# Kernel optimization log

Measured on AMD Instinct MI355X. Metric: run time of the kernel, lower is better.

## Reference

```python
import jax, jax.numpy as jnp
import numpy as np

DIM = 512
HEADS = 8
DIM_HEAD = 64
DIM_INNER = HEADS * DIM_HEAD
FRAC_GRAD = 0.5
SCALE = DIM_HEAD ** -0.5
EPS_CUMPROD = 1e-10
EPS_INV = 1e-8


def setup_inputs() -> dict:
    key = jax.random.key(0)
    ks = jax.random.split(key, 8)
    b, n = 2, 2048
    x = jax.random.normal(ks[0], (b, n, DIM), dtype=jnp.float32)
    gamma = jnp.ones((DIM,), dtype=jnp.float32)
    w_qkv = jax.random.normal(ks[1], (DIM, 3 * DIM_INNER), dtype=jnp.float32) * 0.02
    b_qkv = jnp.zeros((3 * DIM_INNER,), dtype=jnp.float32)
    # to_a: torch init is zeros weight + bias 10; use small random weight and
    # moderate bias so the decay gate is non-trivial for correctness testing
    w_a = jax.random.normal(ks[2], (DIM, DIM_INNER), dtype=jnp.float32) * 0.02
    b_a = jnp.full((DIM_INNER,), 2.0, dtype=jnp.float32)
    w_out = jax.random.normal(ks[3], (DIM_INNER, DIM), dtype=jnp.float32) * 0.02
    b_out = jnp.zeros((DIM,), dtype=jnp.float32)
    return {"x": x, "gamma": gamma, "w_qkv": w_qkv, "b_qkv": b_qkv,
            "w_a": w_a, "b_a": b_a, "w_out": w_out, "b_out": b_out}


def _rms_norm(x, gamma):
    # F.normalize(x, dim=-1) * sqrt(dim) * gamma
    nrm = jnp.linalg.norm(x, axis=-1, keepdims=True)
    return x / jnp.maximum(nrm, 1e-12) * (DIM ** 0.5) * gamma


def _safe_cumprod(t, axis):
    t = jnp.clip(t, EPS_CUMPROD, 1.0)
    return jnp.exp(jnp.cumsum(jnp.log(t), axis=axis))


def reference(x, gamma, w_qkv, b_qkv, w_a, b_a, w_out, b_out):
    b, n, _ = x.shape
    x = _rms_norm(x, gamma)

    qkv = x @ w_qkv + b_qkv  # [b, n, 3*h*d]
    qkv = qkv.reshape(b, n, 3, HEADS, DIM_HEAD).transpose(2, 0, 3, 1, 4)  # [3,b,h,n,d]
    q, k, v = qkv[0], qkv[1], qkv[2]
    q = q * SCALE

    # data-dependent relative-position decay gate
    a = (x @ w_a + b_a).reshape(b, n, HEADS, DIM_HEAD).transpose(0, 2, 1, 3)  # [b,h,n,d]
    a = a * FRAC_GRAD + jax.lax.stop_gradient(a) * (1.0 - FRAC_GRAD)
    a = jax.nn.sigmoid(a)
    a_cum = _safe_cumprod(a, axis=-2)
    a_cum_inv = 1.0 / jnp.maximum(a_cum, EPS_INV)

    q = q * a_cum
    k = k * a_cum_inv

    sim = jnp.einsum('bhid,bhjd->bhij', q, k)
    causal_mask = jnp.triu(jnp.ones((n, n), dtype=bool), k=1)
    attn = jnp.where(causal_mask, 0.0, sim)  # no softmax in decay branch

    out = jnp.einsum('bhij,bhjd->bhid', attn, v)  # [b,h,n,d]
    out = out.transpose(0, 2, 1, 3).reshape(b, n, DIM_INNER)
    return out @ w_out + b_out
```

## Files before the change

kernel.cpp:

```cpp
#include <hip/hip_runtime.h>
#include <hip/hip_cooperative_groups.h>


namespace cg = cooperative_groups;

using s8v   = __attribute__((ext_vector_type(8))) short;
using f32x4 = __attribute__((ext_vector_type(4))) float;

__device__ __forceinline__ unsigned short f2b(float f) {
  unsigned int u = __builtin_bit_cast(unsigned int, f);
  u += 0x7FFFu + ((u >> 16) & 1u);
  return (unsigned short)(u >> 16);
}
__device__ __forceinline__ float b2f(unsigned short b) {
  unsigned int u = ((unsigned int)b) << 16;
  return __builtin_bit_cast(float, u);
}
__device__ __forceinline__ f32x4 mfma16(s8v a, s8v b, f32x4 c) {
  return __builtin_amdgcn_mfma_f32_16x16x32_bf16(a, b, c, 0, 0, 0);
}
__device__ __forceinline__ void gload16(const void* g, void* l) {
  __builtin_amdgcn_global_load_lds(
      (const __attribute__((address_space(1))) void*)g,
      (__attribute__((address_space(3))) void*)l, 16, 0, 0);
}

__device__ __forceinline__ void st_prep(int u, int tid, char* arena,
    const float* __restrict__ x, const float* __restrict__ gamma,
    short* __restrict__ xnb,
    const float* __restrict__ w_qkv, const float* __restrict__ w_a,
    const float* __restrict__ w_out,
    short* __restrict__ wT, short* __restrict__ woT) {
  int lane = tid & 63, wave = tid >> 6;
  if (u < 1024) {
    int row = u * 4 + wave;
    const float4* xp = reinterpret_cast<const float4*>(x + (size_t)row * 512 + lane * 8);
    float4 v0 = xp[0], v1 = xp[1];
    float ss = v0.x*v0.x + v0.y*v0.y + v0.z*v0.z + v0.w*v0.w
             + v1.x*v1.x + v1.y*v1.y + v1.z*v1.z + v1.w*v1.w;
#pragma unroll
    for (int off = 32; off > 0; off >>= 1) ss += __shfl_xor(ss, off, 64);
    float s = 22.627416997969522f / fmaxf(sqrtf(ss), 1e-12f);
    const float* g = gamma + lane * 8;
    float vals[8] = {v0.x, v0.y, v0.z, v0.w, v1.x, v1.y, v1.z, v1.w};
    s8v o;
#pragma unroll
    for (int j = 0; j < 8; ++j) o[j] = (short)f2b(vals[j] * s * g[j]);
    *reinterpret_cast<s8v*>(xnb + (size_t)row * 512 + lane * 8) = o;
  } else {
    float (*t)[33] = reinterpret_cast<float (*)[33]>(arena);
    int id = u - 1024;
    int bx = id % 80, k0 = (id / 80) * 32;
    const float* src; short* dst; int N, n0;
    if (bx < 48)      { src = w_qkv; dst = wT;                      N = 1536; n0 = bx * 32; }
    else if (bx < 64) { src = w_a;   dst = wT + (size_t)1536 * 512; N = 512;  n0 = (bx - 48) * 32; }
    else              { src = w_out; dst = woT;                     N = 512;  n0 = (bx - 64) * 32; }
    int tx = tid & 31, ty = tid >> 5;
    __syncthreads();
#pragma unroll
    for (int i = 0; i < 4; ++i)
      t[ty + 8 * i][tx] = src[(size_t)(k0 + ty + 8 * i) * N + n0 + tx];
    __syncthreads();
#pragma unroll
    for (int i = 0; i < 4; ++i)
      dst[(size_t)(n0 + ty + 8 * i) * 512 + k0 + tx] = (short)f2b(t[tx][ty + 8 * i]);
  }
}

template <int BM, int BN, int FM, int FN>
__device__ __forceinline__ void gemm_core(const short* __restrict__ A,
                                          const short* __restrict__ Bm,
                                          char* LA, char* LB,
                                          int m0, int n0, int tid,
                                          f32x4 (&acc)[FM][FN]) {
  const int lane = tid & 63, wave = tid >> 6;
  const int wr = (wave >> 1) * (BM / 2), wc = (wave & 1) * (BN / 2);
#pragma unroll 1
  for (int t = 0; t < 8; ++t) {
    const int k0 = t * 64;
#pragma unroll
    for (int r = 0; r < BM / 32; ++r) {
      int o = r * 4096 + tid * 16;
      int row = o >> 7;
      int ce = (((o & 127) ^ ((row & 7) << 4)) >> 1);
      gload16(A + (size_t)(m0 + row) * 512 + k0 + ce, LA + o);
    }
#pragma unroll
    for (int r = 0; r < BN / 32; ++r) {
      int o = r * 4096 + tid * 16;
      int row = o >> 7;
      int ce = (((o & 127) ^ ((row & 7) << 4)) >> 1);
      gload16(Bm + (size_t)(n0 + row) * 512 + k0 + ce, LB + o);
    }
    __syncthreads();
#pragma unroll
    for (int kk = 0; kk < 2; ++kk) {
      s8v af[FM], bf[FN];
#pragma unroll
      for (int m = 0; m < FM; ++m) {
        int row = wr + m * 16 + (lane & 15);
        int ad = ((row << 7) + kk * 64 + ((lane >> 4) << 4)) ^ ((row & 7) << 4);
        af[m] = *reinterpret_cast<const s8v*>(LA + ad);
      }
#pragma unroll
      for (int n = 0; n < FN; ++n) {
        int row = wc + n * 16 + (lane & 15);
        int ad = ((row << 7) + kk * 64 + ((lane >> 4) << 4)) ^ ((row & 7) << 4);
        bf[n] = *reinterpret_cast<const s8v*>(LB + ad);
      }
#pragma unroll
      for (int m = 0; m < FM; ++m)
#pragma unroll
        for (int n = 0; n < FN; ++n)
          acc[m][n] = mfma16(af[m], bf[n], acc[m][n]);
    }
    if (t + 1 < 8) __syncthreads();
  }
}

__device__ __forceinline__ void st_gemm0(int vid, int tid, char* arena,
    const short* __restrict__ xnb, const short* __restrict__ wT,
    short* __restrict__ qkvb, const float* __restrict__ b_qkv,
    const float* __restrict__ b_a, float* __restrict__ araw,
    float* __restrict__ csum) {
  const int lane = tid & 63, wave = tid >> 6;
  int xcd = vid & 7, rq = vid >> 3;
  int bx = rq & 15, by = xcd * 4 + (rq >> 4);
  int m0 = by * 128, n0 = bx * 128;
  f32x4 acc[4][4] = {};
  gemm_core<128, 128, 4, 4>(xnb, wT, arena, arena + 16384, m0, n0, tid, acc);
  int wr = (wave >> 1) * 64, wc = (wave & 1) * 64;
  if (n0 < 1536) {
#pragma unroll
    for (int m = 0; m < 4; ++m)
#pragma unroll
      for (int n = 0; n < 4; ++n)
#pragma unroll
        for (int r = 0; r < 4; ++r) {
          int row = m0 + wr + m * 16 + ((lane >> 4) << 2) + r;
          int col = n0 + wc + n * 16 + (lane & 15);
          float v = acc[m][n][r] + b_qkv[col];
          int w = col >> 9, h = (col >> 6) & 7, d = col & 63;
          int b = row >> 11, nn = row & 2047;
          qkvb[((((size_t)(w * 2 + b)) * 8 + h) * 2048 + nn) * 64 + d] = (short)f2b(v);
        }
  } else {
    float cs[4] = {};
    int b = m0 >> 11;
#pragma unroll
    for (int m = 0; m < 4; ++m)
#pragma unroll
      for (int n = 0; n < 4; ++n)
#pragma unroll
        for (int r = 0; r < 4; ++r) {
          int row = m0 + wr + m * 16 + ((lane >> 4) << 2) + r;
          int gc = n0 + wc + n * 16 + (lane & 15) - 1536;
          int h = gc >> 6, d = gc & 63, nn = row & 2047;
          float xv = acc[m][n][r] + b_a[gc];
          araw[((size_t)(b * 8 + h) * 2048 + nn) * 64 + d] = xv;
          float a = 1.f / (1.f + expf(-xv));
          a = fminf(fmaxf(a, 1e-10f), 1.f);
          cs[n] += logf(a);
        }
#pragma unroll
    for (int n = 0; n < 4; ++n) {
      cs[n] += __shfl_xor(cs[n], 16, 64);
      cs[n] += __shfl_xor(cs[n], 32, 64);
    }
    int nsel = lane >> 4;
    float v = (nsel == 0) ? cs[0] : (nsel == 1) ? cs[1] : (nsel == 2) ? cs[2] : cs[3];
    int col = wc + nsel * 16 + (lane & 15);
    int gc = n0 + col - 1536;
    int h = gc >> 6, d = gc & 63;
    int chunkg = ((m0 & 2047) >> 6) + (wave >> 1);
    csum[(((size_t)(b * 8 + h)) * 32 + chunkg) * 64 + d] = v;
  }
}

__device__ __forceinline__ float csum_prefix(const float* __restrict__ csum,
                                             int bh, int chunk, int d) {
  float pre = 0.f;
#pragma unroll
  for (int c = 0; c < 32; ++c) {
    float cv = csum[((size_t)bh * 32 + c) * 64 + d];
    pre += (c < chunk) ? cv : 0.f;
  }
  return pre;
}

__device__ __forceinline__ void st_scan2(int vid, int tid, char* arena,
    const short* __restrict__ qkvb, const float* __restrict__ araw,
    const float* __restrict__ csum, short* __restrict__ q2,
    short* __restrict__ k2, short* __restrict__ vT, short* __restrict__ Sbuf) {
  int chunk = vid & 31, bh = vid >> 5;
  int lane = tid & 63, wave = tid >> 6, d = lane;
  short (*kL)[64] = reinterpret_cast<short (*)[64]>(arena);
  short (*vL)[64] = reinterpret_cast<short (*)[64]>(arena + 8192);
  char* kT  = arena + 16384;
  char* vTl = arena + 24576;
  float (*wsum)[64] = reinterpret_cast<float (*)[64]>(arena + 16384);
  float pre = csum_prefix(csum, bh, chunk, d);
  const float* ap = araw + ((size_t)bh * 2048 + chunk * 64 + wave * 16) * 64 + d;
  float la[16]; float run = 0.f;
#pragma unroll
  for (int rr = 0; rr < 16; ++rr) {
    float xv = ap[rr * 64];
    float a = 1.f / (1.f + expf(-xv));
    a = fminf(fmaxf(a, 1e-10f), 1.f);
    run += logf(a);
    la[rr] = run;
  }
  wsum[wave][d] = run;
  __syncthreads();
#pragma unroll
  for (int w = 0; w < 3; ++w) if (w < wave) pre += wsum[w][d];
  const size_t WS = (size_t)2 * 8 * 2048 * 64;
  size_t base = ((size_t)bh * 2048 + chunk * 64 + wave * 16) * 64 + d;
#pragma unroll 4
  for (int rr = 0; rr < 16; ++rr) {
    int r = wave * 16 + rr;
    float g = expf(pre + la[rr]);
    float gi = 1.f / fmaxf(g, 1e-8f);
    float qv = b2f((unsigned short)qkvb[base + rr * 64]);
    float kv = b2f((unsigned short)qkvb[base + WS + rr * 64]);
    short vb = qkvb[base + 2 * WS + rr * 64];
    q2[base + rr * 64] = (short)f2b(qv * 0.125f * g);
    unsigned short kb = f2b(kv * gi);
    k2[base + rr * 64] = (short)kb;
    kL[r][d] = (short)kb;
    vL[r][d] = vb;
  }
  __syncthreads();
  short* vTrow = vT + ((size_t)bh * 64 + d) * 2048 + chunk * 64;
#pragma unroll
  for (int gg = 0; gg < 2; ++gg) {
    int g8 = wave + gg * 4;
    s8v pk, pv;
#pragma unroll
    for (int j = 0; j < 8; ++j) { pk[j] = kL[g8 * 8 + j][d]; pv[j] = vL[g8 * 8 + j][d]; }
    *reinterpret_cast<s8v*>(vTrow + g8 * 8) = pv;
    int ad = ((d << 7) + g8 * 16) ^ ((d & 7) << 4);
    *reinterpret_cast<s8v*>(kT  + ad) = pk;
    *reinterpret_cast<s8v*>(vTl + ad) = pv;
  }
  __syncthreads();
  f32x4 acc[4] = {};
#pragma unroll
  for (int kk = 0; kk < 2; ++kk) {
    int arow = wave * 16 + (lane & 15);
    int aad = ((arow << 7) + kk * 64 + ((lane >> 4) << 4)) ^ ((arow & 7) << 4);
    s8v av = *reinterpret_cast<const s8v*>(vTl + aad);
#pragma unroll
    for (int n = 0; n < 4; ++n) {
      int brow = n * 16 + (lane & 15);
      int bad = ((brow << 7) + kk * 64 + ((lane >> 4) << 4)) ^ ((brow & 7) << 4);
      acc[n] = mfma16(av, *reinterpret_cast<const s8v*>(kT + bad), acc[n]);
    }
  }
  short* Sp = Sbuf + ((size_t)bh * 32 + chunk) * 4096;
#pragma unroll
  for (int n = 0; n < 4; ++n)
#pragma unroll
    for (int r = 0; r < 4; ++r)
      Sp[(wave * 16 + ((lane >> 4) << 2) + r) * 64 + n * 16 + (lane & 15)] = (short)f2b(acc[n][r]);
}

__device__ __forceinline__ void st_sprefix(int vid, int tid,
    const short* __restrict__ Sbuf, short* __restrict__ Spre) {
  int bh = vid >> 4;
  int e = ((vid & 15) << 8) + tid;
  size_t base = (size_t)bh * 32 * 4096 + e;
  unsigned short v[32];
#pragma unroll
  for (int c = 0; c < 32; ++c)
    v[c] = (unsigned short)Sbuf[base + (size_t)c * 4096];
  float acc = 0.f;
#pragma unroll
  for (int c = 0; c < 32; ++c) {
    Spre[base + (size_t)c * 4096] = (short)f2b(acc);
    acc += b2f(v[c]);
  }
}

__device__ __forceinline__ void st_attnk(int vid, int tid, char* arena,
    const short* __restrict__ q2, const short* __restrict__ k2,
    const short* __restrict__ vT, const short* __restrict__ Spre,
    short* __restrict__ aout) {
  int chunk = vid & 31, bh = vid >> 5;
  int lane = tid & 63, wave = tid >> 6;
  char* LQ = arena;
  char* LK = arena + 8192;
  char* LV = arena + 16384;
  char* LS = arena + 24576;
#pragma unroll
  for (int rr = 0; rr < 2; ++rr) {
    int o = rr * 4096 + tid * 16;
    int row = o >> 7;
    int ce = (((o & 127) ^ ((row & 7) << 4)) >> 1);
    gload16(q2   + ((size_t)bh * 2048 + chunk * 64 + row) * 64 + ce, LQ + o);
    gload16(k2   + ((size_t)bh * 2048 + chunk * 64 + row) * 64 + ce, LK + o);
    gload16(vT   + ((size_t)bh * 64 + row) * 2048 + chunk * 64 + ce, LV + o);
    gload16(Spre + (((size_t)bh * 32 + chunk) * 64 + row) * 64 + ce, LS + o);
  }
  __syncthreads();
  f32x4 accS[4] = {}, accO[4] = {};
#pragma unroll
  for (int kk = 0; kk < 2; ++kk) {
    int arow = wave * 16 + (lane & 15);
    int aad = ((arow << 7) + kk * 64 + ((lane >> 4) << 4)) ^ ((arow & 7) << 4);
    s8v aq = *reinterpret_cast<const s8v*>(LQ + aad);
#pragma unroll
    for (int n = 0; n < 4; ++n) {
      int brow = n * 16 + (lane & 15);
      int bad = ((brow << 7) + kk * 64 + ((lane >> 4) << 4)) ^ ((brow & 7) << 4);
      accS[n] = mfma16(aq, *reinterpret_cast<const s8v*>(LK + bad), accS[n]);
      accO[n] = mfma16(aq, *reinterpret_cast<const s8v*>(LS + bad), accO[n]);
    }
  }
  __syncthreads();
#pragma unroll
  for (int n = 0; n < 4; ++n)
#pragma unroll
    for (int r = 0; r < 4; ++r) {
      int i = wave * 16 + ((lane >> 4) << 2) + r;
      int j = n * 16 + (lane & 15);
      float v = (j <= i) ? accS[n][r] : 0.f;
      int ad = ((i << 7) + (j << 1)) ^ ((i & 7) << 4);
      *reinterpret_cast<short*>(LQ + ad) = (short)f2b(v);
    }
  __syncthreads();
#pragma unroll
  for (int kk = 0; kk < 2; ++kk) {
    int arow = wave * 16 + (lane & 15);
    int aad = ((arow << 7) + kk * 64 + ((lane >> 4) << 4)) ^ ((arow & 7) << 4);
    s8v ap = *reinterpret_cast<const s8v*>(LQ + aad);
#pragma unroll
    for (int n = 0; n < 4; ++n) {
      int brow = n * 16 + (lane & 15);
      int bad = ((brow << 7) + kk * 64 + ((lane >> 4) << 4)) ^ ((brow & 7) << 4);
      accO[n] = mfma16(ap, *reinterpret_cast<const s8v*>(LV + bad), accO[n]);
    }
  }
  int b = bh >> 3, h = bh & 7;
#pragma unroll
  for (int n = 0; n < 4; ++n)
#pragma unroll
    for (int r = 0; r < 4; ++r) {
      int i = wave * 16 + ((lane >> 4) << 2) + r;
      int col = h * 64 + n * 16 + (lane & 15);
      size_t row = (size_t)b * 2048 + chunk * 64 + i;
      aout[row * 512 + col] = (short)f2b(accO[n][r]);
    }
}

__device__ __forceinline__ void st_gemm1(int vid, int tid, char* arena,
    const short* __restrict__ aout, const short* __restrict__ woT,
    float* __restrict__ out, const float* __restrict__ b_out) {
  const int lane = tid & 63, wave = tid >> 6;
  int xcd = vid & 7, rq = vid >> 3;
  int bx = rq & 7, by = xcd * 8 + (rq >> 3);
  int m0 = by * 64, n0 = bx * 64;
  f32x4 acc[2][2] = {};
  gemm_core<64, 64, 2, 2>(aout, woT, arena, arena + 8192, m0, n0, tid, acc);
  int wr = (wave >> 1) * 32, wc = (wave & 1) * 32;
#pragma unroll
  for (int m = 0; m < 2; ++m)
#pragma unroll
    for (int n = 0; n < 2; ++n)
#pragma unroll
      for (int r = 0; r < 4; ++r) {
        int row = m0 + wr + m * 16 + ((lane >> 4) << 2) + r;
        int col = n0 + wc + n * 16 + (lane & 15);
        out[(size_t)row * 512 + col] = acc[m][n][r] + b_out[col];
      }
}

__global__ __launch_bounds__(256, 2) void mega_k(
    const float* __restrict__ x, const float* __restrict__ gamma,
    const float* __restrict__ w_qkv, const float* __restrict__ b_qkv,
    const float* __restrict__ w_a, const float* __restrict__ b_a,
    const float* __restrict__ w_out, const float* __restrict__ b_out,
    float* __restrict__ out,
    short* __restrict__ xnb, short* __restrict__ wT, short* __restrict__ woT,
    short* __restrict__ qkvb, float* __restrict__ araw, float* __restrict__ csum,
    short* __restrict__ Sbuf, short* __restrict__ aout) {
  __shared__ __align__(16) char arena[32768];
  cg::grid_group grid = cg::this_grid();
  const int bid = blockIdx.x, tid = threadIdx.x;
  const int lane = tid & 63, wave = tid >> 6;

  for (int u = bid; u < 2304; u += 512)
    st_prep(u, tid, arena, x, gamma, xnb, w_qkv, w_a, w_out, wT, woT);
  __threadfence(); grid.sync();

  st_gemm0(bid, tid, arena, xnb, wT, qkvb, b_qkv, b_a, araw, csum);
  __threadfence(); grid.sync();

  const int chunk = bid & 31, bh = bid >> 5;
  const int d = lane;
  char* qL  = arena;
  char* kR  = arena + 8192;
  char* kT  = arena + 16384;
  char* vTl = arena + 24576;
  f32x4 accO[4] = {};
  {
    float (*wsum)[64] = reinterpret_cast<float (*)[64]>(kR);
    float pre = csum_prefix(csum, bh, chunk, d);
    const float* ap = araw + ((size_t)bh * 2048 + chunk * 64 + wave * 16) * 64 + d;
    float la[16]; float run = 0.f;
#pragma unroll
    for (int rr = 0; rr < 16; ++rr) {
      float xv = ap[rr * 64];
      float a = 1.f / (1.f + expf(-xv));
      a = fminf(fmaxf(a, 1e-10f), 1.f);
      run += logf(a);
      la[rr] = run;
    }
    wsum[wave][d] = run;
    __syncthreads();
#pragma unroll
    for (int w = 0; w < 3; ++w) if (w < wave) pre += wsum[w][d];
    __syncthreads();
    const size_t WS = (size_t)2 * 8 * 2048 * 64;
    size_t base = ((size_t)bh * 2048 + chunk * 64 + wave * 16) * 64 + d;
#pragma unroll 4
    for (int rr = 0; rr < 16; ++rr) {
      int r = wave * 16 + rr;
      float g = expf(pre + la[rr]);
      float gi = 1.f / fmaxf(g, 1e-8f);
      float qv = b2f((unsigned short)qkvb[base + rr * 64]);
      float kv = b2f((unsigned short)qkvb[base + WS + rr * 64]);
      short vb = qkvb[base + 2 * WS + rr * 64];
      unsigned short qb = f2b(qv * 0.125f * g);
      unsigned short kb = f2b(kv * gi);
      int adr = ((r << 7) + (d << 1)) ^ ((r & 7) << 4);
      *reinterpret_cast<short*>(qL + adr) = (short)qb;
      *reinterpret_cast<short*>(kR + adr) = (short)kb;
      int adt = ((d << 7) + (r << 1)) ^ ((d & 7) << 4);
      *reinterpret_cast<short*>(kT  + adt) = (short)kb;
      *reinterpret_cast<short*>(vTl + adt) = vb;
    }
    __syncthreads();
    f32x4 sacc[4] = {};
#pragma unroll
    for (int kk = 0; kk < 2; ++kk) {
      int arow = wave * 16 + (lane & 15);
      int aad = ((arow << 7) + kk * 64 + ((lane >> 4) << 4)) ^ ((arow & 7) << 4);
      s8v av = *reinterpret_cast<const s8v*>(vTl + aad);
#pragma unroll
      for (int n = 0; n < 4; ++n) {
        int brow = n * 16 + (lane & 15);
        int bad = ((brow << 7) + kk * 64 + ((lane >> 4) << 4)) ^ ((brow & 7) << 4);
        sacc[n] = mfma16(av, *reinterpret_cast<const s8v*>(kT + bad), sacc[n]);
      }
    }
    short* Sp = Sbuf + ((size_t)bh * 32 + chunk) * 4096;
#pragma unroll
    for (int n = 0; n < 4; ++n)
#pragma unroll
      for (int r = 0; r < 4; ++r)
        Sp[(wave * 16 + ((lane >> 4) << 2) + r) * 64 + n * 16 + (lane & 15)] = (short)f2b(sacc[n][r]);
    f32x4 accS[4] = {};
#pragma unroll
    for (int kk = 0; kk < 2; ++kk) {
      int arow = wave * 16 + (lane & 15);
      int aad = ((arow << 7) + kk * 64 + ((lane >> 4) << 4)) ^ ((arow & 7) << 4);
      s8v aq = *reinterpret_cast<const s8v*>(qL + aad);
#pragma unroll
      for (int n = 0; n < 4; ++n) {
        int brow = n * 16 + (lane & 15);
        int bad = ((brow << 7) + kk * 64 + ((lane >> 4) << 4)) ^ ((brow & 7) << 4);
        accS[n] = mfma16(aq, *reinterpret_cast<const s8v*>(kR + bad), accS[n]);
      }
    }
    __syncthreads();
#pragma unroll
    for (int n = 0; n < 4; ++n)
#pragma unroll
      for (int r = 0; r < 4; ++r) {
        int i = wave * 16 + ((lane >> 4) << 2) + r;
        int j = n * 16 + (lane & 15);
        float v = (j <= i) ? accS[n][r] : 0.f;
        int ad = ((i << 7) + (j << 1)) ^ ((i & 7) << 4);
        *reinterpret_cast<short*>(kT + ad) = (short)f2b(v);
      }
    __syncthreads();
#pragma unroll
    for (int kk = 0; kk < 2; ++kk) {
      int arow = wave * 16 + (lane & 15);
      int aad = ((arow << 7) + kk * 64 + ((lane >> 4) << 4)) ^ ((arow & 7) << 4);
      s8v ap = *reinterpret_cast<const s8v*>(kT + aad);
#pragma unroll
      for (int n = 0; n < 4; ++n) {
        int brow = n * 16 + (lane & 15);
        int bad = ((brow << 7) + kk * 64 + ((lane >> 4) << 4)) ^ ((brow & 7) << 4);
        accO[n] = mfma16(ap, *reinterpret_cast<const s8v*>(vTl + bad), accO[n]);
      }
    }
  }
  __threadfence(); grid.sync();

  {
    char* LS = kR;
    int srow = tid >> 2, scol0 = (tid & 3) * 16;
    const short* Sb = Sbuf + (size_t)bh * 32 * 4096 + srow * 64 + scol0;
    float acc0[8] = {}, acc1[8] = {};
#pragma unroll
    for (int c = 0; c < 32; ++c) {
      if (c < chunk) {
        s8v v0 = *reinterpret_cast<const s8v*>(Sb + (size_t)c * 4096);
        s8v v1 = *reinterpret_cast<const s8v*>(Sb + (size_t)c * 4096 + 8);
#pragma unroll
        for (int j = 0; j < 8; ++j) {
          acc0[j] += b2f((unsigned short)v0[j]);
          acc1[j] += b2f((unsigned short)v1[j]);
        }
      }
    }
    s8v o0, o1;
#pragma unroll
    for (int j = 0; j < 8; ++j) {
      o0[j] = (short)f2b(acc0[j]);
      o1[j] = (short)f2b(acc1[j]);
    }
    int byte0 = (srow << 7) + (scol0 << 1);
    int sw = (srow & 7) << 4;
    *reinterpret_cast<s8v*>(LS + ((byte0)      ^ sw)) = o0;
    *reinterpret_cast<s8v*>(LS + ((byte0 + 16) ^ sw)) = o1;
    __syncthreads();
#pragma unroll
    for (int kk = 0; kk < 2; ++kk) {
      int arow = wave * 16 + (lane & 15);
      int aad = ((arow << 7) + kk * 64 + ((lane >> 4) << 4)) ^ ((arow & 7) << 4);
      s8v aq = *reinterpret_cast<const s8v*>(qL + aad);
#pragma unroll
      for (int n = 0; n < 4; ++n) {
        int brow = n * 16 + (lane & 15);
        int bad = ((brow << 7) + kk * 64 + ((lane >> 4) << 4)) ^ ((brow & 7) << 4);
        accO[n] = mfma16(aq, *reinterpret_cast<const s8v*>(LS + bad), accO[n]);
      }
    }
    int b = bh >> 3, h = bh & 7;
#pragma unroll
    for (int n = 0; n < 4; ++n)
#pragma unroll
      for (int r = 0; r < 4; ++r) {
        int i = wave * 16 + ((lane >> 4) << 2) + r;
        int col = h * 64 + n * 16 + (lane & 15);
        size_t row = (size_t)b * 2048 + chunk * 64 + i;
        aout[row * 512 + col] = (short)f2b(accO[n][r]);
      }
  }
  __threadfence(); grid.sync();

  st_gemm1(bid, tid, arena, aout, woT, out, b_out);
}

__global__ __launch_bounds__(256) void prep_k(const float* x, const float* gamma,
    short* xnb, const float* w_qkv, const float* w_a, const float* w_out,
    short* wT, short* woT) {
  __shared__ __align__(16) char arena[4224];
  st_prep(blockIdx.x, threadIdx.x, arena, x, gamma, xnb, w_qkv, w_a, w_out, wT, woT);
}
__global__ __launch_bounds__(256) void gemm0_k(const short* xnb, const short* wT,
    short* qkvb, const float* b_qkv, const float* b_a, float* araw, float* csum) {
  __shared__ __align__(16) char arena[32768];
  st_gemm0(blockIdx.x, threadIdx.x, arena, xnb, wT, qkvb, b_qkv, b_a, araw, csum);
}
__global__ __launch_bounds__(256) void scan2_k(const short* qkvb, const float* araw,
    const float* csum, short* q2, short* k2, short* vT, short* Sbuf) {
  __shared__ __align__(16) char arena[32768];
  st_scan2(blockIdx.x, threadIdx.x, arena, qkvb, araw, csum, q2, k2, vT, Sbuf);
}
__global__ __launch_bounds__(256) void sprefix_k(const short* Sbuf, short* Spre) {
  st_sprefix(blockIdx.x, threadIdx.x, Sbuf, Spre);
}
__global__ __launch_bounds__(256) void attnk_k(const short* q2, const short* k2,
    const short* vT, const short* Spre, short* aout) {
  __shared__ __align__(16) char arena[32768];
  st_attnk(blockIdx.x, threadIdx.x, arena, q2, k2, vT, Spre, aout);
}
__global__ __launch_bounds__(256) void gemm1_k(const short* aout, const short* woT,
    float* out, const float* b_out) {
  __shared__ __align__(16) char arena[16384];
  st_gemm1(blockIdx.x, threadIdx.x, arena, aout, woT, out, b_out);
}

extern "C" void kernel_launch(void* const* d_in, const int* in_sizes, int n_in,
                              void* d_out, int out_size, void* d_ws, size_t ws_size,
                              hipStream_t stream) {
  const float* x     = (const float*)d_in[0];
  const float* gamma = (const float*)d_in[1];
  const float* w_qkv = (const float*)d_in[2];
  const float* b_qkv = (const float*)d_in[3];
  const float* w_a   = (const float*)d_in[4];
  const float* b_a   = (const float*)d_in[5];
  const float* w_out = (const float*)d_in[6];
  const float* b_out = (const float*)d_in[7];
  float* out = (float*)d_out;
  char* ws = (char*)d_ws;

  const size_t MB = 1u << 20;
  short* xnb  = (short*)(ws);
  short* wT   = (short*)(ws + 4  * MB);
  short* woT  = (short*)(ws + 6  * MB);
  short* qkvb = (short*)(ws + 7  * MB);
  float* araw = (float*)(ws + 19 * MB);
  float* csum = (float*)(ws + 27 * MB);
  short* Sbuf = (short*)(ws + 28 * MB);
  short* aout = (short*)(ws + 32 * MB);
  short* Spre = (short*)(ws + 36 * MB);
  short* q2   = (short*)(ws + 40 * MB);
  short* k2   = (short*)(ws + 44 * MB);
  short* vT   = (short*)(ws + 48 * MB);

  int dev = 0; (void)hipGetDevice(&dev);
  int coop = 0;
  (void)hipDeviceGetAttribute(&coop, hipDeviceAttributeCooperativeLaunch, dev);
  int nb = 0;
  (void)hipOccupancyMaxActiveBlocksPerMultiprocessor(&nb, mega_k, 256, 0);

  hipError_t err = hipErrorUnknown;
  if (coop && nb >= 2) {
    void* args[] = {&x, &gamma, &w_qkv, &b_qkv, &w_a, &b_a, &w_out, &b_out,
                    &out, &xnb, &wT, &woT, &qkvb, &araw, &csum,
                    &Sbuf, &aout};
    err = hipLaunchCooperativeKernel((void*)mega_k, dim3(512), dim3(256), args, 0, stream);
  }
  if (err != hipSuccess) {
    prep_k   <<<2304, 256, 0, stream>>>(x, gamma, xnb, w_qkv, w_a, w_out, wT, woT);
    gemm0_k  <<<512,  256, 0, stream>>>(xnb, wT, qkvb, b_qkv, b_a, araw, csum);
    scan2_k  <<<512,  256, 0, stream>>>(qkvb, araw, csum, q2, k2, vT, Sbuf);
    sprefix_k<<<256,  256, 0, stream>>>(Sbuf, Spre);
    attnk_k  <<<512,  256, 0, stream>>>(q2, k2, vT, Spre, aout);
    gemm1_k  <<<512,  256, 0, stream>>>(aout, woT, out, b_out);
  }
}
```

Baseline: 61.45 us.

## Double cooperative grid to 1024 blocks with smaller GEMM tiles

The cooperative mega-kernel now launches 1024 blocks of 256 threads with a four-blocks-per-CU launch bound, instead of 512. To fill the larger grid, the QKV/decay-gate GEMM shrinks to 128x64 tiles and the output GEMM to 64x32 tiles, each using a 4x1 wave layout. The per-chunk log-sum of the gate is now reduced across waves through shared memory. The aim is more parallel work per CU in the GEMM stages, at the cost of higher register pressure, costlier grid syncs, and middle stages that map two blocks onto each of the 512 work units.

```diff
diff --git a/kernel.cpp b/kernel.cpp
--- a/kernel.cpp
+++ b/kernel.cpp
@@ -67,14 +67,15 @@
   }
 }
 
-template <int BM, int BN, int FM, int FN>
+template <int BM, int BN, int WR, int WC>
 __device__ __forceinline__ void gemm_core(const short* __restrict__ A,
                                           const short* __restrict__ Bm,
                                           char* LA, char* LB,
                                           int m0, int n0, int tid,
-                                          f32x4 (&acc)[FM][FN]) {
+                                          f32x4 (&acc)[BM / WR / 16][BN / WC / 16]) {
+  constexpr int WM = BM / WR, WN = BN / WC, FM = WM / 16, FN = WN / 16;
   const int lane = tid & 63, wave = tid >> 6;
-  const int wr = (wave >> 1) * (BM / 2), wc = (wave & 1) * (BN / 2);
+  const int wr = (wave / WC) * WM, wc = (wave % WC) * WN;
 #pragma unroll 1
   for (int t = 0; t < 8; ++t) {
     const int k0 = t * 64;
@@ -125,36 +126,38 @@
     float* __restrict__ csum) {
   const int lane = tid & 63, wave = tid >> 6;
   int xcd = vid & 7, rq = vid >> 3;
-  int bx = rq & 15, by = xcd * 4 + (rq >> 4);
-  int m0 = by * 128, n0 = bx * 128;
-  f32x4 acc[4][4] = {};
-  gemm_core<128, 128, 4, 4>(xnb, wT, arena, arena + 16384, m0, n0, tid, acc);
-  int wr = (wave >> 1) * 64, wc = (wave & 1) * 64;
+  int bx = rq & 31, by = xcd * 4 + (rq >> 5);
+  int m0 = by * 128, n0 = bx * 64;
+  f32x4 acc[2][4] = {};
+  gemm_core<128, 64, 4, 1>(xnb, wT, arena, arena + 16384, m0, n0, tid, acc);
+  int wr = wave * 32;
   if (n0 < 1536) {
 #pragma unroll
-    for (int m = 0; m < 4; ++m)
+    for (int m = 0; m < 2; ++m)
 #pragma unroll
       for (int n = 0; n < 4; ++n)
 #pragma unroll
         for (int r = 0; r < 4; ++r) {
           int row = m0 + wr + m * 16 + ((lane >> 4) << 2) + r;
-          int col = n0 + wc + n * 16 + (lane & 15);
+          int col = n0 + n * 16 + (lane & 15);
           float v = acc[m][n][r] + b_qkv[col];
           int w = col >> 9, h = (col >> 6) & 7, d = col & 63;
           int b = row >> 11, nn = row & 2047;
           qkvb[((((size_t)(w * 2 + b)) * 8 + h) * 2048 + nn) * 64 + d] = (short)f2b(v);
         }
   } else {
+    __syncthreads();
+    float (*WSUM)[64] = reinterpret_cast<float (*)[64]>(arena);
     float cs[4] = {};
     int b = m0 >> 11;
 #pragma unroll
-    for (int m = 0; m < 4; ++m)
+    for (int m = 0; m < 2; ++m)
 #pragma unroll
       for (int n = 0; n < 4; ++n)
 #pragma unroll
         for (int r = 0; r < 4; ++r) {
           int row = m0 + wr + m * 16 + ((lane >> 4) << 2) + r;
-          int gc = n0 + wc + n * 16 + (lane & 15) - 1536;
+          int gc = n0 + n * 16 + (lane & 15) - 1536;
           int h = gc >> 6, d = gc & 63, nn = row & 2047;
           float xv = acc[m][n][r] + b_a[gc];
           araw[((size_t)(b * 8 + h) * 2048 + nn) * 64 + d] = xv;
@@ -167,13 +170,18 @@
       cs[n] += __shfl_xor(cs[n], 16, 64);
       cs[n] += __shfl_xor(cs[n], 32, 64);
     }
-    int nsel = lane >> 4;
-    float v = (nsel == 0) ? cs[0] : (nsel == 1) ? cs[1] : (nsel == 2) ? cs[2] : cs[3];
-    int col = wc + nsel * 16 + (lane & 15);
-    int gc = n0 + col - 1536;
-    int h = gc >> 6, d = gc & 63;
-    int chunkg = ((m0 & 2047) >> 6) + (wave >> 1);
-    csum[(((size_t)(b * 8 + h)) * 32 + chunkg) * 64 + d] = v;
+    if (lane < 16) {
+#pragma unroll
+      for (int n = 0; n < 4; ++n) WSUM[wave][n * 16 + lane] = cs[n];
+    }
+    __syncthreads();
+    if (tid < 128) {
+      int cl = tid >> 6, col = tid & 63;
+      float s = WSUM[2 * cl][col] + WSUM[2 * cl + 1][col];
+      int h = (n0 - 1536) >> 6;
+      int chunkg = ((m0 & 2047) >> 6) + cl;
+      csum[(((size_t)(b * 8 + h)) * 32 + chunkg) * 64 + col] = s;
+    }
   }
 }
 
@@ -358,24 +366,22 @@
     float* __restrict__ out, const float* __restrict__ b_out) {
   const int lane = tid & 63, wave = tid >> 6;
   int xcd = vid & 7, rq = vid >> 3;
-  int bx = rq & 7, by = xcd * 8 + (rq >> 3);
-  int m0 = by * 64, n0 = bx * 64;
-  f32x4 acc[2][2] = {};
-  gemm_core<64, 64, 2, 2>(aout, woT, arena, arena + 8192, m0, n0, tid, acc);
-  int wr = (wave >> 1) * 32, wc = (wave & 1) * 32;
-#pragma unroll
-  for (int m = 0; m < 2; ++m)
-#pragma unroll
-    for (int n = 0; n < 2; ++n)
-#pragma unroll
-      for (int r = 0; r < 4; ++r) {
-        int row = m0 + wr + m * 16 + ((lane >> 4) << 2) + r;
-        int col = n0 + wc + n * 16 + (lane & 15);
-        out[(size_t)row * 512 + col] = acc[m][n][r] + b_out[col];
-      }
-}
-
-__global__ __launch_bounds__(256, 2) void mega_k(
+  int bx = rq & 15, by = xcd * 8 + (rq >> 4);
+  int m0 = by * 64, n0 = bx * 32;
+  f32x4 acc[1][2] = {};
+  gemm_core<64, 32, 4, 1>(aout, woT, arena, arena + 8192, m0, n0, tid, acc);
+  int wr = wave * 16;
+#pragma unroll
+  for (int n = 0; n < 2; ++n)
+#pragma unroll
+    for (int r = 0; r < 4; ++r) {
+      int row = m0 + wr + ((lane >> 4) << 2) + r;
+      int col = n0 + n * 16 + (lane & 15);
+      out[(size_t)row * 512 + col] = acc[0][n][r] + b_out[col];
+    }
+}
+
+__global__ __launch_bounds__(256, 4) void mega_k(
     const float* __restrict__ x, const float* __restrict__ gamma,
     const float* __restrict__ w_qkv, const float* __restrict__ b_qkv,
     const float* __restrict__ w_a, const float* __restrict__ b_a,
@@ -389,14 +395,15 @@
   const int bid = blockIdx.x, tid = threadIdx.x;
   const int lane = tid & 63, wave = tid >> 6;
 
-  for (int u = bid; u < 2304; u += 512)
+  for (int u = bid; u < 2304; u += 1024)
     st_prep(u, tid, arena, x, gamma, xnb, w_qkv, w_a, w_out, wT, woT);
   __threadfence(); grid.sync();
 
   st_gemm0(bid, tid, arena, xnb, wT, qkvb, b_qkv, b_a, araw, csum);
   __threadfence(); grid.sync();
 
-  const int chunk = bid & 31, bh = bid >> 5;
+  const int unit = bid & 511;
+  const int chunk = unit & 31, bh = unit >> 5;
   const int d = lane;
   char* qL  = arena;
   char* kR  = arena + 8192;
@@ -564,7 +571,7 @@
 }
 __global__ __launch_bounds__(256) void gemm0_k(const short* xnb, const short* wT,
     short* qkvb, const float* b_qkv, const float* b_a, float* araw, float* csum) {
-  __shared__ __align__(16) char arena[32768];
+  __shared__ __align__(16) char arena[24576];
   st_gemm0(blockIdx.x, threadIdx.x, arena, xnb, wT, qkvb, b_qkv, b_a, araw, csum);
 }
 __global__ __launch_bounds__(256) void scan2_k(const short* qkvb, const float* araw,
@@ -582,7 +589,7 @@
 }
 __global__ __launch_bounds__(256) void gemm1_k(const short* aout, const short* woT,
     float* out, const float* b_out) {
-  __shared__ __align__(16) char arena[16384];
+  __shared__ __align__(16) char arena[12288];
   st_gemm1(blockIdx.x, threadIdx.x, arena, aout, woT, out, b_out);
 }
 
@@ -621,18 +628,18 @@
   (void)hipOccupancyMaxActiveBlocksPerMultiprocessor(&nb, mega_k, 256, 0);
 
   hipError_t err = hipErrorUnknown;
-  if (coop && nb >= 2) {
+  if (coop && nb >= 4) {
     void* args[] = {&x, &gamma, &w_qkv, &b_qkv, &w_a, &b_a, &w_out, &b_out,
                     &out, &xnb, &wT, &woT, &qkvb, &araw, &csum,
                     &Sbuf, &aout};
-    err = hipLaunchCooperativeKernel((void*)mega_k, dim3(512), dim3(256), args, 0, stream);
+    err = hipLaunchCooperativeKernel((void*)mega_k, dim3(1024), dim3(256), args, 0, stream);
   }
   if (err != hipSuccess) {
     prep_k   <<<2304, 256, 0, stream>>>(x, gamma, xnb, w_qkv, w_a, w_out, wT, woT);
-    gemm0_k  <<<512,  256, 0, stream>>>(xnb, wT, qkvb, b_qkv, b_a, araw, csum);
+    gemm0_k  <<<1024, 256, 0, stream>>>(xnb, wT, qkvb, b_qkv, b_a, araw, csum);
     scan2_k  <<<512,  256, 0, stream>>>(qkvb, araw, csum, q2, k2, vT, Sbuf);
     sprefix_k<<<256,  256, 0, stream>>>(Sbuf, Spre);
     attnk_k  <<<512,  256, 0, stream>>>(q2, k2, vT, Spre, aout);
-    gemm1_k  <<<512,  256, 0, stream>>>(aout, woT, out, b_out);
-  }
-}
+    gemm1_k  <<<1024, 256, 0, stream>>>(aout, woT, out, b_out);
+  }
+}
```

After: 59.68 us. 2.9% less time.
